# Performance work log

Measured on AMD Instinct MI355X. Metric: run time of the kernel, lower is better.

Reference implementation:

```python
import jax, jax.numpy as jnp
import numpy as np

N_NODES = 50000
N_EDGES = 800000
STATE_DIM = 128
H1 = 96
H2 = 64


def setup_inputs() -> dict:
    key = jax.random.key(0)
    ks = jax.random.split(key, 10)
    x = jax.random.normal(ks[0], (N_NODES, STATE_DIM), dtype=jnp.float32)
    edge_index = jax.random.randint(ks[1], (2, N_EDGES), 0, N_NODES, dtype=jnp.int64)
    # GCNConv weight [in, out] and bias
    W1 = jax.random.normal(ks[2], (STATE_DIM, H1), dtype=jnp.float32) / np.sqrt(STATE_DIM)
    b1 = jnp.zeros((H1,), dtype=jnp.float32)
    lw1 = jax.random.normal(ks[3], (H1, H1), dtype=jnp.float32) / np.sqrt(H1)
    lb1 = jax.random.normal(ks[4], (H1,), dtype=jnp.float32) * 0.01
    lw2 = jax.random.normal(ks[5], (H1, H2), dtype=jnp.float32) / np.sqrt(H1)
    lb2 = jax.random.normal(ks[6], (H2,), dtype=jnp.float32) * 0.01
    lw3 = jax.random.normal(ks[7], (H2, 1), dtype=jnp.float32) / np.sqrt(H2)
    lb3 = jax.random.normal(ks[8], (1,), dtype=jnp.float32) * 0.01
    return {"x": x, "edge_index": edge_index, "W1": W1, "b1": b1,
            "lw1": lw1, "lb1": lb1, "lw2": lw2, "lb2": lb2, "lw3": lw3, "lb3": lb3}


def reference(x, edge_index, W1, b1, lw1, lb1, lw2, lb2, lw3, lb3):
    N = x.shape[0]
    loop = jnp.arange(N, dtype=edge_index.dtype)
    src = jnp.concatenate([edge_index[0], loop])
    dst = jnp.concatenate([edge_index[1], loop])
    deg = jax.ops.segment_sum(jnp.ones_like(dst, dtype=x.dtype), dst, num_segments=N)
    dinv = jnp.where(deg > 0, jax.lax.rsqrt(jnp.maximum(deg, 1.0)), 0.0)
    norm = dinv[src] * dinv[dst]  # [E+N]
    h = x @ W1  # [N, H1] transform before propagation
    agg = jax.ops.segment_sum(h[src] * norm[:, None], dst, num_segments=N) + b1
    out = jax.nn.relu(agg)            # [N, H1]
    g = jnp.sum(out, axis=0)          # sum pooling over nodes -> [H1]
    g = jax.nn.relu(g @ lw1 + lb1)
    g = jax.nn.relu(g @ lw2 + lb2)
    return g @ lw3 + lb3              # [1]
```

## Files before the change

### kernel.cpp

```cpp
#include <hip/hip_runtime.h>
#include <stdint.h>

#define N_NODES 50000
#define N_EDGES 800000
#define D_IN 128
#define H1 96
#define H2 64
#define GEMM_NODES 32
#define GEMM_BLOCKS ((N_NODES + GEMM_NODES - 1) / GEMM_NODES)
#define COUNT_BLOCKS 256
#define SCAN_BLK 256
#define N_SBLK ((N_NODES + SCAN_BLK - 1) / SCAN_BLK)
#define SCAT_BLOCKS 2048
#define SCALE_BLOCKS 512

__global__ __launch_bounds__(256) void k1_gemm_count(const float* __restrict__ x,
                                                     const float* __restrict__ W1,
                                                     float* __restrict__ h,
                                                     const int* __restrict__ dst,
                                                     int* __restrict__ deg) {
    __shared__ float sW[D_IN * H1];
    __shared__ float sx[GEMM_NODES * D_IN];
    int tid = threadIdx.x;

    if (blockIdx.x < GEMM_BLOCKS) {
        for (int i = tid; i < D_IN * H1 / 4; i += 256)
            ((float4*)sW)[i] = ((const float4*)W1)[i];

        int base = blockIdx.x * GEMM_NODES;
        const float4* x4 = (const float4*)x;
        for (int i = tid; i < GEMM_NODES * D_IN / 4; i += 256) {
            int n = base + i / (D_IN / 4);
            if (n < N_NODES) ((float4*)sx)[i] = x4[(size_t)base * (D_IN / 4) + i];
        }
        __syncthreads();

        int fg = tid & 31;
        int ng = tid >> 5;

        float acc[4][3];
#pragma unroll
        for (int i = 0; i < 4; ++i)
#pragma unroll
            for (int j = 0; j < 3; ++j) acc[i][j] = 0.0f;

#pragma unroll 4
        for (int k = 0; k < D_IN; ++k) {
            float w0 = sW[k * H1 + fg];
            float w1 = sW[k * H1 + fg + 32];
            float w2 = sW[k * H1 + fg + 64];
#pragma unroll
            for (int i = 0; i < 4; ++i) {
                float xv = sx[(ng * 4 + i) * D_IN + k];
                acc[i][0] = fmaf(xv, w0, acc[i][0]);
                acc[i][1] = fmaf(xv, w1, acc[i][1]);
                acc[i][2] = fmaf(xv, w2, acc[i][2]);
            }
        }

#pragma unroll
        for (int i = 0; i < 4; ++i) {
            int n = base + ng * 4 + i;
            if (n < N_NODES) {
                h[(size_t)n * H1 + fg]      = acc[i][0];
                h[(size_t)n * H1 + fg + 32] = acc[i][1];
                h[(size_t)n * H1 + fg + 64] = acc[i][2];
            }
        }
    } else {
        int bid = blockIdx.x - GEMM_BLOCKS;
        int gid = bid * 256 + tid;
        int stride = COUNT_BLOCKS * 256;
        const int4* d4 = (const int4*)dst;
        for (int i = gid; i < N_EDGES / 4; i += stride) {
            int4 d = d4[i];
            atomicAdd(&deg[d.x], 1);
            atomicAdd(&deg[d.y], 1);
            atomicAdd(&deg[d.z], 1);
            atomicAdd(&deg[d.w], 1);
        }
    }
}

__global__ __launch_bounds__(SCAN_BLK) void deg_part_kernel(const int* __restrict__ deg,
                                                            int* __restrict__ block_sums) {
    __shared__ int s[SCAN_BLK];
    int t = threadIdx.x;
    int i = blockIdx.x * SCAN_BLK + t;
    s[t] = (i < N_NODES) ? deg[i] : 0;
    __syncthreads();
    for (int off = SCAN_BLK / 2; off > 0; off >>= 1) {
        if (t < off) s[t] += s[t + off];
        __syncthreads();
    }
    if (t == 0) block_sums[blockIdx.x] = s[0];
}

__global__ __launch_bounds__(SCAN_BLK) void block_scan_kernel(int* __restrict__ block_sums) {
    __shared__ int s[SCAN_BLK];
    int t = threadIdx.x;
    int v = (t < N_SBLK) ? block_sums[t] : 0;
    s[t] = v;
    __syncthreads();
    for (int off = 1; off < SCAN_BLK; off <<= 1) {
        int u = (t >= off) ? s[t - off] : 0;
        __syncthreads();
        s[t] += u;
        __syncthreads();
    }
    if (t < N_SBLK) block_sums[t] = s[t] - v;
}

__global__ __launch_bounds__(SCAN_BLK) void deg_scan_kernel(const int* __restrict__ deg,
                                                            const int* __restrict__ block_off,
                                                            int* __restrict__ row_start,
                                                            int* __restrict__ cursor,
                                                            float* __restrict__ dinv) {
    __shared__ int s[SCAN_BLK];
    int t = threadIdx.x;
    int i = blockIdx.x * SCAN_BLK + t;
    int v = (i < N_NODES) ? deg[i] : 0;
    s[t] = v;
    __syncthreads();
    for (int off = 1; off < SCAN_BLK; off <<= 1) {
        int u = (t >= off) ? s[t - off] : 0;
        __syncthreads();
        s[t] += u;
        __syncthreads();
    }
    int excl = s[t] - v + block_off[blockIdx.x];
    if (i < N_NODES) {
        row_start[i] = excl;
        cursor[i] = excl;
        dinv[i] = rsqrtf((float)v + 1.0f);
    }
    if (i == 0) row_start[N_NODES] = N_EDGES;
}

__global__ __launch_bounds__(256) void k3_scatter_scale(const int* __restrict__ src,
                                                        const int* __restrict__ dst,
                                                        int* __restrict__ cursor,
                                                        int* __restrict__ sorted_src,
                                                        float* __restrict__ h,
                                                        const float* __restrict__ dinv) {
    int tid = threadIdx.x;
    if (blockIdx.x < SCAT_BLOCKS) {
        int gid = blockIdx.x * 256 + tid;
        int stride = SCAT_BLOCKS * 256;
        for (int e = gid; e < N_EDGES; e += stride) {
            int d = dst[e];
            int pos = atomicAdd(&cursor[d], 1);
            sorted_src[pos] = src[e];
        }
    } else {
        int bid = blockIdx.x - SCAT_BLOCKS;
        int gid = bid * 256 + tid;
        int stride = SCALE_BLOCKS * 256;
        float4* h4 = (float4*)h;
        const int TOT = N_NODES * (H1 / 4);
        for (int i = gid; i < TOT; i += stride) {
            int n = i / (H1 / 4);
            float dv = dinv[n];
            float4 v = h4[i];
            v.x *= dv; v.y *= dv; v.z *= dv; v.w *= dv;
            h4[i] = v;
        }
    }
}

__global__ __launch_bounds__(256) void agg_pool_kernel(const float* __restrict__ hs,
                                                       const int* __restrict__ row_start,
                                                       const int* __restrict__ sorted_src,
                                                       const float* __restrict__ dinv,
                                                       const float* __restrict__ b1,
                                                       float* __restrict__ g) {
    int tid = threadIdx.x;
    int grp = tid >> 7;
    int f = tid & 127;
    bool act = f < H1;
    float bf = act ? b1[f] : 0.0f;
    float gacc = 0.0f;

    for (int n = blockIdx.x * 2 + grp; n < N_NODES; n += gridDim.x * 2) {
        float acc = act ? hs[(size_t)n * H1 + f] : 0.0f;
        int e = row_start[n];
        int eend = row_start[n + 1];
        for (; e + 4 <= eend; e += 4) {
            int s0 = sorted_src[e];
            int s1 = sorted_src[e + 1];
            int s2 = sorted_src[e + 2];
            int s3 = sorted_src[e + 3];
            if (act) {
                float v0 = hs[(size_t)s0 * H1 + f];
                float v1 = hs[(size_t)s1 * H1 + f];
                float v2 = hs[(size_t)s2 * H1 + f];
                float v3 = hs[(size_t)s3 * H1 + f];
                acc += (v0 + v1) + (v2 + v3);
            }
        }
        for (; e < eend; ++e) {
            int s = sorted_src[e];
            if (act) acc += hs[(size_t)s * H1 + f];
        }
        if (act) gacc += fmaxf(fmaf(dinv[n], acc, bf), 0.0f);
    }

    __shared__ float sg[H1];
    if (grp == 0 && act) sg[f] = gacc;
    __syncthreads();
    if (grp == 1 && act) atomicAdd(&sg[f], gacc);
    __syncthreads();
    if (grp == 0 && act) atomicAdd(&g[f], sg[f]);
}

__global__ __launch_bounds__(256) void mlp_kernel(const float* __restrict__ g,
                           const float* __restrict__ lw1, const float* __restrict__ lb1,
                           const float* __restrict__ lw2, const float* __restrict__ lb2,
                           const float* __restrict__ lw3, const float* __restrict__ lb3,
                           float* __restrict__ out) {
    __shared__ float slw1[H1 * H1];
    __shared__ float slw2[H1 * H2];
    __shared__ float slw3[H2];
    __shared__ float sg[H1], v1[H1], v2[H2];
    int t = threadIdx.x;
    for (int i = t; i < H1 * H1 / 4; i += 256)
        ((float4*)slw1)[i] = ((const float4*)lw1)[i];
    for (int i = t; i < H1 * H2 / 4; i += 256)
        ((float4*)slw2)[i] = ((const float4*)lw2)[i];
    if (t < H2) slw3[t] = lw3[t];
    if (t < H1) sg[t] = g[t];
    __syncthreads();
    if (t < H1) {
        float a = lb1[t];
#pragma unroll 8
        for (int k = 0; k < H1; ++k) a = fmaf(sg[k], slw1[k * H1 + t], a);
        v1[t] = fmaxf(a, 0.0f);
    }
    __syncthreads();
    if (t < H2) {
        float a = lb2[t];
#pragma unroll 8
        for (int k = 0; k < H1; ++k) a = fmaf(v1[k], slw2[k * H2 + t], a);
        v2[t] = fmaxf(a, 0.0f);
    }
    __syncthreads();
    if (t == 0) {
        float a = lb3[0];
#pragma unroll 8
        for (int k = 0; k < H2; ++k) a = fmaf(v2[k], slw3[k], a);
        out[0] = a;
    }
}

extern "C" void kernel_launch(void* const* d_in, const int* in_sizes, int n_in,
                              void* d_out, int out_size, void* d_ws, size_t ws_size,
                              hipStream_t stream) {
    const float* x   = (const float*)d_in[0];
    const int*   ei  = (const int*)d_in[1];
    const float* W1  = (const float*)d_in[2];
    const float* b1  = (const float*)d_in[3];
    const float* lw1 = (const float*)d_in[4];
    const float* lb1 = (const float*)d_in[5];
    const float* lw2 = (const float*)d_in[6];
    const float* lb2 = (const float*)d_in[7];
    const float* lw3 = (const float*)d_in[8];
    const float* lb3 = (const float*)d_in[9];
    float* out = (float*)d_out;

    const int* src = ei;
    const int* dst = ei + N_EDGES;

    char* ws = (char*)d_ws;
    size_t off = 0;
    auto alloc = [&](size_t bytes) {
        char* p = ws + off;
        off = (off + bytes + 255) & ~(size_t)255;
        return p;
    };
    int*   deg        = (int*)alloc((size_t)N_NODES * sizeof(int));
    float* g          = (float*)alloc((size_t)H1 * sizeof(float));
    float* dinv       = (float*)alloc((size_t)N_NODES * sizeof(float));
    int*   row_start  = (int*)alloc((size_t)(N_NODES + 1) * sizeof(int));
    int*   cursor     = (int*)alloc((size_t)N_NODES * sizeof(int));
    int*   block_sums = (int*)alloc((size_t)N_SBLK * sizeof(int));
    int*   sorted_src = (int*)alloc((size_t)N_EDGES * sizeof(int));
    float* h          = (float*)alloc((size_t)N_NODES * H1 * sizeof(float));
    (void)ws_size;

    hipMemsetAsync(deg, 0, (char*)(g + H1) - (char*)deg, stream);

    k1_gemm_count<<<GEMM_BLOCKS + COUNT_BLOCKS, 256, 0, stream>>>(x, W1, h, dst, deg);

    deg_part_kernel<<<N_SBLK, SCAN_BLK, 0, stream>>>(deg, block_sums);
    block_scan_kernel<<<1, SCAN_BLK, 0, stream>>>(block_sums);
    deg_scan_kernel<<<N_SBLK, SCAN_BLK, 0, stream>>>(deg, block_sums, row_start, cursor, dinv);

    k3_scatter_scale<<<SCAT_BLOCKS + SCALE_BLOCKS, 256, 0, stream>>>(src, dst, cursor, sorted_src, h, dinv);

    agg_pool_kernel<<<2048, 256, 0, stream>>>(h, row_start, sorted_src, dinv, b1, g);

    mlp_kernel<<<1, 256, 0, stream>>>(g, lw1, lb1, lw2, lb2, lw3, lb3, out);
}
```

Measured before the change: 248.3 us.

## Shard CSR by source range so aggregation gathers hit a cache-sized slice

Edges are bucketed by (src>>13, dst), which gives 7 source shards of 8192 nodes. Each shard's slice of h is about 3 MB, small enough to stay in cache while it is read. The aggregation kernel now walks its fixed set of nodes shard by shard and keeps per-node accumulators in registers, so concurrent gathers share one shard's rows and L2 hits should rise. In exchange the degree, scan and cursor arrays grow sevenfold, the block scan gets larger, a separate dinv kernel is added, and each node's row_start is read once per shard.

```diff
diff --git a/kernel.cpp b/kernel.cpp
--- a/kernel.cpp
+++ b/kernel.cpp
@@ -6,17 +6,23 @@
 #define D_IN 128
 #define H1 96
 #define H2 64
+#define N_SHARD 7
+#define NB (N_SHARD * N_NODES)
 #define GEMM_NODES 32
 #define GEMM_BLOCKS ((N_NODES + GEMM_NODES - 1) / GEMM_NODES)
 #define COUNT_BLOCKS 256
 #define SCAN_BLK 256
-#define N_SBLK ((N_NODES + SCAN_BLK - 1) / SCAN_BLK)
+#define NB_SBLK ((NB + SCAN_BLK - 1) / SCAN_BLK)
 #define SCAT_BLOCKS 2048
 #define SCALE_BLOCKS 512
+#define AGG_BLOCKS 2048
+#define NGROUPS (AGG_BLOCKS * 2)
+#define NPG ((N_NODES + NGROUPS - 1) / NGROUPS)
 
 __global__ __launch_bounds__(256) void k1_gemm_count(const float* __restrict__ x,
                                                      const float* __restrict__ W1,
                                                      float* __restrict__ h,
+                                                     const int* __restrict__ src,
                                                      const int* __restrict__ dst,
                                                      int* __restrict__ deg) {
     __shared__ float sW[D_IN * H1];
@@ -71,13 +77,15 @@
         int bid = blockIdx.x - GEMM_BLOCKS;
         int gid = bid * 256 + tid;
         int stride = COUNT_BLOCKS * 256;
-        const int4* d4 = (const int4*)dst;
+        const int4* s4p = (const int4*)src;
+        const int4* d4p = (const int4*)dst;
         for (int i = gid; i < N_EDGES / 4; i += stride) {
-            int4 d = d4[i];
-            atomicAdd(&deg[d.x], 1);
-            atomicAdd(&deg[d.y], 1);
-            atomicAdd(&deg[d.z], 1);
-            atomicAdd(&deg[d.w], 1);
+            int4 sv = s4p[i];
+            int4 dv = d4p[i];
+            atomicAdd(&deg[(sv.x >> 13) * N_NODES + dv.x], 1);
+            atomicAdd(&deg[(sv.y >> 13) * N_NODES + dv.y], 1);
+            atomicAdd(&deg[(sv.z >> 13) * N_NODES + dv.z], 1);
+            atomicAdd(&deg[(sv.w >> 13) * N_NODES + dv.w], 1);
         }
     }
 }
@@ -87,7 +95,7 @@
     __shared__ int s[SCAN_BLK];
     int t = threadIdx.x;
     int i = blockIdx.x * SCAN_BLK + t;
-    s[t] = (i < N_NODES) ? deg[i] : 0;
+    s[t] = (i < NB) ? deg[i] : 0;
     __syncthreads();
     for (int off = SCAN_BLK / 2; off > 0; off >>= 1) {
         if (t < off) s[t] += s[t + off];
@@ -96,30 +104,34 @@
     if (t == 0) block_sums[blockIdx.x] = s[0];
 }
 
-__global__ __launch_bounds__(SCAN_BLK) void block_scan_kernel(int* __restrict__ block_sums) {
-    __shared__ int s[SCAN_BLK];
+__global__ __launch_bounds__(1024) void block_scan_kernel(int* __restrict__ block_sums) {
+    __shared__ int s[1024];
     int t = threadIdx.x;
-    int v = (t < N_SBLK) ? block_sums[t] : 0;
-    s[t] = v;
-    __syncthreads();
-    for (int off = 1; off < SCAN_BLK; off <<= 1) {
+    int i0 = t * 2;
+    int v0 = (i0 < NB_SBLK) ? block_sums[i0] : 0;
+    int v1 = (i0 + 1 < NB_SBLK) ? block_sums[i0 + 1] : 0;
+    int sum = v0 + v1;
+    s[t] = sum;
+    __syncthreads();
+    for (int off = 1; off < 1024; off <<= 1) {
         int u = (t >= off) ? s[t - off] : 0;
         __syncthreads();
         s[t] += u;
         __syncthreads();
     }
-    if (t < N_SBLK) block_sums[t] = s[t] - v;
+    int excl = s[t] - sum;
+    if (i0 < NB_SBLK) block_sums[i0] = excl;
+    if (i0 + 1 < NB_SBLK) block_sums[i0 + 1] = excl + v0;
 }
 
 __global__ __launch_bounds__(SCAN_BLK) void deg_scan_kernel(const int* __restrict__ deg,
                                                             const int* __restrict__ block_off,
                                                             int* __restrict__ row_start,
-                                                            int* __restrict__ cursor,
-                                                            float* __restrict__ dinv) {
+                                                            int* __restrict__ cursor) {
     __shared__ int s[SCAN_BLK];
     int t = threadIdx.x;
     int i = blockIdx.x * SCAN_BLK + t;
-    int v = (i < N_NODES) ? deg[i] : 0;
+    int v = (i < NB) ? deg[i] : 0;
     s[t] = v;
     __syncthreads();
     for (int off = 1; off < SCAN_BLK; off <<= 1) {
@@ -129,12 +141,21 @@
         __syncthreads();
     }
     int excl = s[t] - v + block_off[blockIdx.x];
-    if (i < N_NODES) {
+    if (i < NB) {
         row_start[i] = excl;
         cursor[i] = excl;
-        dinv[i] = rsqrtf((float)v + 1.0f);
-    }
-    if (i == 0) row_start[N_NODES] = N_EDGES;
+    }
+    if (i == 0) row_start[NB] = N_EDGES;
+}
+
+__global__ void dinv_kernel(const int* __restrict__ deg, float* __restrict__ dinv) {
+    int n = blockIdx.x * 256 + threadIdx.x;
+    if (n < N_NODES) {
+        int tot = 1;
+#pragma unroll
+        for (int s = 0; s < N_SHARD; ++s) tot += deg[s * N_NODES + n];
+        dinv[n] = rsqrtf((float)tot);
+    }
 }
 
 __global__ __launch_bounds__(256) void k3_scatter_scale(const int* __restrict__ src,
@@ -148,9 +169,11 @@
         int gid = blockIdx.x * 256 + tid;
         int stride = SCAT_BLOCKS * 256;
         for (int e = gid; e < N_EDGES; e += stride) {
+            int sval = src[e];
             int d = dst[e];
-            int pos = atomicAdd(&cursor[d], 1);
-            sorted_src[pos] = src[e];
+            int b = (sval >> 13) * N_NODES + d;
+            int pos = atomicAdd(&cursor[b], 1);
+            sorted_src[pos] = sval;
         }
     } else {
         int bid = blockIdx.x - SCAT_BLOCKS;
@@ -179,30 +202,51 @@
     int f = tid & 127;
     bool act = f < H1;
     float bf = act ? b1[f] : 0.0f;
+    int gid = blockIdx.x * 2 + grp;
+
+    float acc[NPG];
+#pragma unroll
+    for (int i = 0; i < NPG; ++i) {
+        int n = gid + i * NGROUPS;
+        acc[i] = (act && n < N_NODES) ? hs[(size_t)n * H1 + f] : 0.0f;
+    }
+
+    for (int s = 0; s < N_SHARD; ++s) {
+        const int* rs = row_start + s * N_NODES;
+#pragma unroll
+        for (int i = 0; i < NPG; ++i) {
+            int n = gid + i * NGROUPS;
+            if (n < N_NODES) {
+                int e = rs[n];
+                int ee = rs[n + 1];
+                float a = acc[i];
+                for (; e + 4 <= ee; e += 4) {
+                    int s0 = sorted_src[e];
+                    int s1 = sorted_src[e + 1];
+                    int s2 = sorted_src[e + 2];
+                    int s3 = sorted_src[e + 3];
+                    if (act) {
+                        float v0 = hs[(size_t)s0 * H1 + f];
+                        float v1 = hs[(size_t)s1 * H1 + f];
+                        float v2 = hs[(size_t)s2 * H1 + f];
+                        float v3 = hs[(size_t)s3 * H1 + f];
+                        a += (v0 + v1) + (v2 + v3);
+                    }
+                }
+                for (; e < ee; ++e) {
+                    int ss = sorted_src[e];
+                    if (act) a += hs[(size_t)ss * H1 + f];
+                }
+                acc[i] = a;
+            }
+        }
+    }
+
     float gacc = 0.0f;
-
-    for (int n = blockIdx.x * 2 + grp; n < N_NODES; n += gridDim.x * 2) {
-        float acc = act ? hs[(size_t)n * H1 + f] : 0.0f;
-        int e = row_start[n];
-        int eend = row_start[n + 1];
-        for (; e + 4 <= eend; e += 4) {
-            int s0 = sorted_src[e];
-            int s1 = sorted_src[e + 1];
-            int s2 = sorted_src[e + 2];
-            int s3 = sorted_src[e + 3];
-            if (act) {
-                float v0 = hs[(size_t)s0 * H1 + f];
-                float v1 = hs[(size_t)s1 * H1 + f];
-                float v2 = hs[(size_t)s2 * H1 + f];
-                float v3 = hs[(size_t)s3 * H1 + f];
-                acc += (v0 + v1) + (v2 + v3);
-            }
-        }
-        for (; e < eend; ++e) {
-            int s = sorted_src[e];
-            if (act) acc += hs[(size_t)s * H1 + f];
-        }
-        if (act) gacc += fmaxf(fmaf(dinv[n], acc, bf), 0.0f);
+#pragma unroll
+    for (int i = 0; i < NPG; ++i) {
+        int n = gid + i * NGROUPS;
+        if (act && n < N_NODES) gacc += fmaxf(fmaf(dinv[n], acc[i], bf), 0.0f);
     }
 
     __shared__ float sg[H1];
@@ -277,27 +321,28 @@
         off = (off + bytes + 255) & ~(size_t)255;
         return p;
     };
-    int*   deg        = (int*)alloc((size_t)N_NODES * sizeof(int));
+    int*   deg        = (int*)alloc((size_t)NB * sizeof(int));
     float* g          = (float*)alloc((size_t)H1 * sizeof(float));
     float* dinv       = (float*)alloc((size_t)N_NODES * sizeof(float));
-    int*   row_start  = (int*)alloc((size_t)(N_NODES + 1) * sizeof(int));
-    int*   cursor     = (int*)alloc((size_t)N_NODES * sizeof(int));
-    int*   block_sums = (int*)alloc((size_t)N_SBLK * sizeof(int));
+    int*   row_start  = (int*)alloc((size_t)(NB + 1) * sizeof(int));
+    int*   cursor     = (int*)alloc((size_t)NB * sizeof(int));
+    int*   block_sums = (int*)alloc((size_t)NB_SBLK * sizeof(int));
     int*   sorted_src = (int*)alloc((size_t)N_EDGES * sizeof(int));
     float* h          = (float*)alloc((size_t)N_NODES * H1 * sizeof(float));
     (void)ws_size;
 
     hipMemsetAsync(deg, 0, (char*)(g + H1) - (char*)deg, stream);
 
-    k1_gemm_count<<<GEMM_BLOCKS + COUNT_BLOCKS, 256, 0, stream>>>(x, W1, h, dst, deg);
-
-    deg_part_kernel<<<N_SBLK, SCAN_BLK, 0, stream>>>(deg, block_sums);
-    block_scan_kernel<<<1, SCAN_BLK, 0, stream>>>(block_sums);
-    deg_scan_kernel<<<N_SBLK, SCAN_BLK, 0, stream>>>(deg, block_sums, row_start, cursor, dinv);
+    k1_gemm_count<<<GEMM_BLOCKS + COUNT_BLOCKS, 256, 0, stream>>>(x, W1, h, src, dst, deg);
+
+    deg_part_kernel<<<NB_SBLK, SCAN_BLK, 0, stream>>>(deg, block_sums);
+    block_scan_kernel<<<1, 1024, 0, stream>>>(block_sums);
+    deg_scan_kernel<<<NB_SBLK, SCAN_BLK, 0, stream>>>(deg, block_sums, row_start, cursor);
+    dinv_kernel<<<(N_NODES + 255) / 256, 256, 0, stream>>>(deg, dinv);
 
     k3_scatter_scale<<<SCAT_BLOCKS + SCALE_BLOCKS, 256, 0, stream>>>(src, dst, cursor, sorted_src, h, dinv);
 
-    agg_pool_kernel<<<2048, 256, 0, stream>>>(h, row_start, sorted_src, dinv, b1, g);
+    agg_pool_kernel<<<AGG_BLOCKS, 256, 0, stream>>>(h, row_start, sorted_src, dinv, b1, g);
 
     mlp_kernel<<<1, 256, 0, stream>>>(g, lw1, lb1, lw2, lb2, lw3, lb3, out);
 }
```

New measurement: 389.2 us. +56.7%, slower.

## Fuse dinv scaling into GEMM and co-schedule GEMM with CSR scatter

Applied to the files above, without the earlier changes.

The GEMM moves after the degree scan so it can multiply by dinv on store, which removes the separate read-modify-write pass over h. The GEMM now runs in the same launch as the CSR scatter, and the degree count gets its own kernel with more blocks. W1 is read directly from global memory instead of being staged in shared memory, and the h rows are padded to 128 floats so gathers line up with 512-byte rows. The scatter path uses int4 loads and nontemporal stores. In exchange, the padding adds memory traffic and the uncached W1 reads may add latency to the GEMM inner loop.

```diff
diff --git a/kernel.cpp b/kernel.cpp
--- a/kernel.cpp
+++ b/kernel.cpp
@@ -5,29 +5,115 @@
 #define N_EDGES 800000
 #define D_IN 128
 #define H1 96
+#define HP 128
 #define H2 64
 #define GEMM_NODES 32
 #define GEMM_BLOCKS ((N_NODES + GEMM_NODES - 1) / GEMM_NODES)
-#define COUNT_BLOCKS 256
+#define COUNT_BLOCKS 1024
 #define SCAN_BLK 256
 #define N_SBLK ((N_NODES + SCAN_BLK - 1) / SCAN_BLK)
-#define SCAT_BLOCKS 2048
-#define SCALE_BLOCKS 512
-
-__global__ __launch_bounds__(256) void k1_gemm_count(const float* __restrict__ x,
-                                                     const float* __restrict__ W1,
-                                                     float* __restrict__ h,
-                                                     const int* __restrict__ dst,
-                                                     int* __restrict__ deg) {
-    __shared__ float sW[D_IN * H1];
+#define SCAT_BLOCKS 782
+#define AGG_BLOCKS 2048
+
+__global__ void count_deg_kernel(const int* __restrict__ dst, int* __restrict__ deg) {
+    int gid = blockIdx.x * 256 + threadIdx.x;
+    int stride = COUNT_BLOCKS * 256;
+    const int4* d4 = (const int4*)dst;
+    for (int i = gid; i < N_EDGES / 4; i += stride) {
+        int4 d = d4[i];
+        atomicAdd(&deg[d.x], 1);
+        atomicAdd(&deg[d.y], 1);
+        atomicAdd(&deg[d.z], 1);
+        atomicAdd(&deg[d.w], 1);
+    }
+}
+
+__global__ __launch_bounds__(SCAN_BLK) void deg_part_kernel(const int* __restrict__ deg,
+                                                            int* __restrict__ block_sums) {
+    __shared__ int s[SCAN_BLK];
+    int t = threadIdx.x;
+    int i = blockIdx.x * SCAN_BLK + t;
+    s[t] = (i < N_NODES) ? deg[i] : 0;
+    __syncthreads();
+    for (int off = SCAN_BLK / 2; off > 0; off >>= 1) {
+        if (t < off) s[t] += s[t + off];
+        __syncthreads();
+    }
+    if (t == 0) block_sums[blockIdx.x] = s[0];
+}
+
+__global__ __launch_bounds__(SCAN_BLK) void block_scan_kernel(int* __restrict__ block_sums) {
+    __shared__ int s[SCAN_BLK];
+    int t = threadIdx.x;
+    int v = (t < N_SBLK) ? block_sums[t] : 0;
+    s[t] = v;
+    __syncthreads();
+    for (int off = 1; off < SCAN_BLK; off <<= 1) {
+        int u = (t >= off) ? s[t - off] : 0;
+        __syncthreads();
+        s[t] += u;
+        __syncthreads();
+    }
+    if (t < N_SBLK) block_sums[t] = s[t] - v;
+}
+
+__global__ __launch_bounds__(SCAN_BLK) void deg_scan_kernel(const int* __restrict__ deg,
+                                                            const int* __restrict__ block_off,
+                                                            int* __restrict__ row_start,
+                                                            int* __restrict__ cursor,
+                                                            float* __restrict__ dinv) {
+    __shared__ int s[SCAN_BLK];
+    int t = threadIdx.x;
+    int i = blockIdx.x * SCAN_BLK + t;
+    int v = (i < N_NODES) ? deg[i] : 0;
+    s[t] = v;
+    __syncthreads();
+    for (int off = 1; off < SCAN_BLK; off <<= 1) {
+        int u = (t >= off) ? s[t - off] : 0;
+        __syncthreads();
+        s[t] += u;
+        __syncthreads();
+    }
+    int excl = s[t] - v + block_off[blockIdx.x];
+    if (i < N_NODES) {
+        row_start[i] = excl;
+        cursor[i] = excl;
+        dinv[i] = rsqrtf((float)v + 1.0f);
+    }
+    if (i == 0) row_start[N_NODES] = N_EDGES;
+}
+
+__global__ __launch_bounds__(256) void k2_scatter_gemm(const int* __restrict__ src,
+                                                       const int* __restrict__ dst,
+                                                       int* __restrict__ cursor,
+                                                       int* __restrict__ sorted_src,
+                                                       const float* __restrict__ x,
+                                                       const float* __restrict__ W1,
+                                                       const float* __restrict__ dinv,
+                                                       float* __restrict__ hs) {
     __shared__ float sx[GEMM_NODES * D_IN];
     int tid = threadIdx.x;
 
-    if (blockIdx.x < GEMM_BLOCKS) {
-        for (int i = tid; i < D_IN * H1 / 4; i += 256)
-            ((float4*)sW)[i] = ((const float4*)W1)[i];
-
-        int base = blockIdx.x * GEMM_NODES;
+    if (blockIdx.x < SCAT_BLOCKS) {
+        int gid = blockIdx.x * 256 + tid;
+        int stride = SCAT_BLOCKS * 256;
+        const int4* s4p = (const int4*)src;
+        const int4* d4p = (const int4*)dst;
+        for (int i = gid; i < N_EDGES / 4; i += stride) {
+            int4 sv = s4p[i];
+            int4 dv = d4p[i];
+            int p0 = atomicAdd(&cursor[dv.x], 1);
+            int p1 = atomicAdd(&cursor[dv.y], 1);
+            int p2 = atomicAdd(&cursor[dv.z], 1);
+            int p3 = atomicAdd(&cursor[dv.w], 1);
+            __builtin_nontemporal_store(sv.x, &sorted_src[p0]);
+            __builtin_nontemporal_store(sv.y, &sorted_src[p1]);
+            __builtin_nontemporal_store(sv.z, &sorted_src[p2]);
+            __builtin_nontemporal_store(sv.w, &sorted_src[p3]);
+        }
+    } else {
+        int gblk = blockIdx.x - SCAT_BLOCKS;
+        int base = gblk * GEMM_NODES;
         const float4* x4 = (const float4*)x;
         for (int i = tid; i < GEMM_NODES * D_IN / 4; i += 256) {
             int n = base + i / (D_IN / 4);
@@ -46,9 +132,9 @@
 
 #pragma unroll 4
         for (int k = 0; k < D_IN; ++k) {
-            float w0 = sW[k * H1 + fg];
-            float w1 = sW[k * H1 + fg + 32];
-            float w2 = sW[k * H1 + fg + 64];
+            float w0 = W1[k * H1 + fg];
+            float w1 = W1[k * H1 + fg + 32];
+            float w2 = W1[k * H1 + fg + 64];
 #pragma unroll
             for (int i = 0; i < 4; ++i) {
                 float xv = sx[(ng * 4 + i) * D_IN + k];
@@ -62,108 +148,11 @@
         for (int i = 0; i < 4; ++i) {
             int n = base + ng * 4 + i;
             if (n < N_NODES) {
-                h[(size_t)n * H1 + fg]      = acc[i][0];
-                h[(size_t)n * H1 + fg + 32] = acc[i][1];
-                h[(size_t)n * H1 + fg + 64] = acc[i][2];
+                float dv = dinv[n];
+                hs[(size_t)n * HP + fg]      = acc[i][0] * dv;
+                hs[(size_t)n * HP + fg + 32] = acc[i][1] * dv;
+                hs[(size_t)n * HP + fg + 64] = acc[i][2] * dv;
             }
-        }
-    } else {
-        int bid = blockIdx.x - GEMM_BLOCKS;
-        int gid = bid * 256 + tid;
-        int stride = COUNT_BLOCKS * 256;
-        const int4* d4 = (const int4*)dst;
-        for (int i = gid; i < N_EDGES / 4; i += stride) {
-            int4 d = d4[i];
-            atomicAdd(&deg[d.x], 1);
-            atomicAdd(&deg[d.y], 1);
-            atomicAdd(&deg[d.z], 1);
-            atomicAdd(&deg[d.w], 1);
-        }
-    }
-}
-
-__global__ __launch_bounds__(SCAN_BLK) void deg_part_kernel(const int* __restrict__ deg,
-                                                            int* __restrict__ block_sums) {
-    __shared__ int s[SCAN_BLK];
-    int t = threadIdx.x;
-    int i = blockIdx.x * SCAN_BLK + t;
-    s[t] = (i < N_NODES) ? deg[i] : 0;
-    __syncthreads();
-    for (int off = SCAN_BLK / 2; off > 0; off >>= 1) {
-        if (t < off) s[t] += s[t + off];
-        __syncthreads();
-    }
-    if (t == 0) block_sums[blockIdx.x] = s[0];
-}
-
-__global__ __launch_bounds__(SCAN_BLK) void block_scan_kernel(int* __restrict__ block_sums) {
-    __shared__ int s[SCAN_BLK];
-    int t = threadIdx.x;
-    int v = (t < N_SBLK) ? block_sums[t] : 0;
-    s[t] = v;
-    __syncthreads();
-    for (int off = 1; off < SCAN_BLK; off <<= 1) {
-        int u = (t >= off) ? s[t - off] : 0;
-        __syncthreads();
-        s[t] += u;
-        __syncthreads();
-    }
-    if (t < N_SBLK) block_sums[t] = s[t] - v;
-}
-
-__global__ __launch_bounds__(SCAN_BLK) void deg_scan_kernel(const int* __restrict__ deg,
-                                                            const int* __restrict__ block_off,
-                                                            int* __restrict__ row_start,
-                                                            int* __restrict__ cursor,
-                                                            float* __restrict__ dinv) {
-    __shared__ int s[SCAN_BLK];
-    int t = threadIdx.x;
-    int i = blockIdx.x * SCAN_BLK + t;
-    int v = (i < N_NODES) ? deg[i] : 0;
-    s[t] = v;
-    __syncthreads();
-    for (int off = 1; off < SCAN_BLK; off <<= 1) {
-        int u = (t >= off) ? s[t - off] : 0;
-        __syncthreads();
-        s[t] += u;
-        __syncthreads();
-    }
-    int excl = s[t] - v + block_off[blockIdx.x];
-    if (i < N_NODES) {
-        row_start[i] = excl;
-        cursor[i] = excl;
-        dinv[i] = rsqrtf((float)v + 1.0f);
-    }
-    if (i == 0) row_start[N_NODES] = N_EDGES;
-}
-
-__global__ __launch_bounds__(256) void k3_scatter_scale(const int* __restrict__ src,
-                                                        const int* __restrict__ dst,
-                                                        int* __restrict__ cursor,
-                                                        int* __restrict__ sorted_src,
-                                                        float* __restrict__ h,
-                                                        const float* __restrict__ dinv) {
-    int tid = threadIdx.x;
-    if (blockIdx.x < SCAT_BLOCKS) {
-        int gid = blockIdx.x * 256 + tid;
-        int stride = SCAT_BLOCKS * 256;
-        for (int e = gid; e < N_EDGES; e += stride) {
-            int d = dst[e];
-            int pos = atomicAdd(&cursor[d], 1);
-            sorted_src[pos] = src[e];
-        }
-    } else {
-        int bid = blockIdx.x - SCAT_BLOCKS;
-        int gid = bid * 256 + tid;
-        int stride = SCALE_BLOCKS * 256;
-        float4* h4 = (float4*)h;
-        const int TOT = N_NODES * (H1 / 4);
-        for (int i = gid; i < TOT; i += stride) {
-            int n = i / (H1 / 4);
-            float dv = dinv[n];
-            float4 v = h4[i];
-            v.x *= dv; v.y *= dv; v.z *= dv; v.w *= dv;
-            h4[i] = v;
         }
     }
 }
@@ -182,7 +171,7 @@
     float gacc = 0.0f;
 
     for (int n = blockIdx.x * 2 + grp; n < N_NODES; n += gridDim.x * 2) {
-        float acc = act ? hs[(size_t)n * H1 + f] : 0.0f;
+        float acc = act ? hs[(size_t)n * HP + f] : 0.0f;
         int e = row_start[n];
         int eend = row_start[n + 1];
         for (; e + 4 <= eend; e += 4) {
@@ -191,16 +180,16 @@
             int s2 = sorted_src[e + 2];
             int s3 = sorted_src[e + 3];
             if (act) {
-                float v0 = hs[(size_t)s0 * H1 + f];
-                float v1 = hs[(size_t)s1 * H1 + f];
-                float v2 = hs[(size_t)s2 * H1 + f];
-                float v3 = hs[(size_t)s3 * H1 + f];
+                float v0 = hs[(size_t)s0 * HP + f];
+                float v1 = hs[(size_t)s1 * HP + f];
+                float v2 = hs[(size_t)s2 * HP + f];
+                float v3 = hs[(size_t)s3 * HP + f];
                 acc += (v0 + v1) + (v2 + v3);
             }
         }
         for (; e < eend; ++e) {
             int s = sorted_src[e];
-            if (act) acc += hs[(size_t)s * H1 + f];
+            if (act) acc += hs[(size_t)s * HP + f];
         }
         if (act) gacc += fmaxf(fmaf(dinv[n], acc, bf), 0.0f);
     }
@@ -284,20 +273,20 @@
     int*   cursor     = (int*)alloc((size_t)N_NODES * sizeof(int));
     int*   block_sums = (int*)alloc((size_t)N_SBLK * sizeof(int));
     int*   sorted_src = (int*)alloc((size_t)N_EDGES * sizeof(int));
-    float* h          = (float*)alloc((size_t)N_NODES * H1 * sizeof(float));
+    float* hs         = (float*)alloc((size_t)N_NODES * HP * sizeof(float));
     (void)ws_size;
 
     hipMemsetAsync(deg, 0, (char*)(g + H1) - (char*)deg, stream);
 
-    k1_gemm_count<<<GEMM_BLOCKS + COUNT_BLOCKS, 256, 0, stream>>>(x, W1, h, dst, deg);
-
+    count_deg_kernel<<<COUNT_BLOCKS, 256, 0, stream>>>(dst, deg);
     deg_part_kernel<<<N_SBLK, SCAN_BLK, 0, stream>>>(deg, block_sums);
     block_scan_kernel<<<1, SCAN_BLK, 0, stream>>>(block_sums);
     deg_scan_kernel<<<N_SBLK, SCAN_BLK, 0, stream>>>(deg, block_sums, row_start, cursor, dinv);
 
-    k3_scatter_scale<<<SCAT_BLOCKS + SCALE_BLOCKS, 256, 0, stream>>>(src, dst, cursor, sorted_src, h, dinv);
-
-    agg_pool_kernel<<<2048, 256, 0, stream>>>(h, row_start, sorted_src, dinv, b1, g);
+    k2_scatter_gemm<<<SCAT_BLOCKS + GEMM_BLOCKS, 256, 0, stream>>>(src, dst, cursor, sorted_src,
+                                                                   x, W1, dinv, hs);
+
+    agg_pool_kernel<<<AGG_BLOCKS, 256, 0, stream>>>(hs, row_start, sorted_src, dinv, b1, g);
 
     mlp_kernel<<<1, 256, 0, stream>>>(g, lw1, lb1, lw2, lb2, lw3, lb3, out);
 }
```

Measured after the change: 261.7 us. 1.05x slower.
